# Optimization experiments

Measured on AMD Instinct MI355X. Metric: run time of the kernel, lower is better.

The kernel has to match this reference:

```python
import jax, jax.numpy as jnp
import numpy as np

N_NODES, N_EDGES, N_REL, F_DIM, N_HEAD, N_LAYERS = 20000, 100000, 1000, 128, 4, 4
NEG_SLOPE = 0.2  # PyG GATv2Conv default negative_slope


def _gatv2_layer(x, ea_full, src, dst, Wl, bl, Wr, br, We, att, bias):
    # x: [N, F]; ea_full: [Etot, F] edge attrs (incl. self-loop rows)
    N = x.shape[0]
    H, C = att.shape  # heads, out-dim per head
    xl = (x @ Wl + bl).reshape(N, H, C)          # source-side projection
    xr = (x @ Wr + br).reshape(N, H, C)          # target-side projection
    ee = (ea_full @ We).reshape(-1, H, C)        # [Etot, H, C] edge embedding
    # GATv2 scoring: leaky_relu(x_i + x_j + e) . att
    e = jax.nn.leaky_relu(xl[src] + xr[dst] + ee, NEG_SLOPE)
    logits = jnp.einsum('ehc,hc->eh', e, att)    # [Etot, H]
    # segment softmax over edges grouped by destination node
    m = jax.ops.segment_max(logits, dst, num_segments=N)
    p = jnp.exp(logits - m[dst])
    denom = jax.ops.segment_sum(p, dst, num_segments=N)
    alpha = p / denom[dst]                       # [Etot, H]
    out = jax.ops.segment_sum(alpha[:, :, None] * xl[src], dst, num_segments=N)
    return out.mean(axis=1) + bias               # concat=False -> head mean


def setup_inputs() -> dict:
    key = jax.random.key(0)
    ks = jax.random.split(key, 12)
    N, E, R, F, H, L = N_NODES, N_EDGES, N_REL, F_DIM, N_HEAD, N_LAYERS
    HC = H * F
    s = 1.0 / np.sqrt(F)
    return {
        'x': jax.random.normal(ks[0], (N, F), jnp.float32),
        'edge_index': jax.random.randint(ks[1], (2, E), 0, N, dtype=jnp.int32),
        'relations': jax.random.normal(ks[2], (R, F), jnp.float32),
        'relation_index': jax.random.randint(ks[3], (E,), 0, R, dtype=jnp.int32),
        'Wl': jax.random.normal(ks[4], (L, F, HC), jnp.float32) * s,
        'bl': jnp.zeros((L, HC), jnp.float32),
        'Wr': jax.random.normal(ks[5], (L, F, HC), jnp.float32) * s,
        'br': jnp.zeros((L, HC), jnp.float32),
        'We': jax.random.normal(ks[6], (L, F, HC), jnp.float32) * s,
        'att': jax.random.normal(ks[7], (L, H, F), jnp.float32) * s,
        'bias': jnp.zeros((L, F), jnp.float32),
    }


def reference(x, edge_index, relations, relation_index, Wl, bl, Wr, br, We, att, bias):
    N = x.shape[0]
    sl = jnp.arange(N, dtype=edge_index.dtype)
    src = jnp.concatenate([edge_index[0], sl])   # add_self_loops=True
    dst = jnp.concatenate([edge_index[1], sl])
    ea = relations[relation_index]               # [E, F]
    # self-loop edge_attr uses fill_value='mean' (PyG default)
    ea_mean = ea.mean(axis=0)
    ea_full = jnp.concatenate([ea, jnp.broadcast_to(ea_mean, (N, ea.shape[1]))])
    h = x
    for l in range(N_LAYERS):
        h = _gatv2_layer(h, ea_full, src, dst, Wl[l], bl[l], Wr[l], br[l], We[l], att[l], bias[l])
    return (h, relations)
```

## Files before the change

kernel.cpp:

```cpp
#include <hip/hip_runtime.h>
#include <hip/hip_bf16.h>

#define N_NODES   20000
#define N_EDGES   100000
#define N_REL     1000
#define F_DIM     128
#define N_HEAD    4
#define HC        512
#define HC2       256
#define N_LAYERS  4
#define REL_EXT_ROWS 1008
#define NEG_SLOPE 0.2f
#define PROJ_NODE_X 79

typedef __attribute__((ext_vector_type(8))) short short8;
typedef __attribute__((ext_vector_type(4))) float floatx4;

__device__ __forceinline__ float loadIn(const void* p, size_t i, int f32) {
    if (f32) return ((const float*)p)[i];
    union { unsigned int u; float f; } c;
    c.u = ((unsigned int)((const unsigned short*)p)[i]) << 16;
    return c.f;
}

__device__ __forceinline__ unsigned short f2bf(float v) {
    __hip_bfloat16 b = __float2bfloat16(v);
    return *(unsigned short*)&b;
}

__device__ __forceinline__ void unpack2(unsigned int u, float& lo, float& hi) {
    union { unsigned int u; float f; } a, b;
    a.u = u << 16;
    b.u = u & 0xFFFF0000u;
    lo = a.f; hi = b.f;
}

__device__ __forceinline__ void unpack8(uint4 v, float* f) {
    unpack2(v.x, f[0], f[1]);
    unpack2(v.y, f[2], f[3]);
    unpack2(v.z, f[4], f[5]);
    unpack2(v.w, f[6], f[7]);
}

__device__ __forceinline__ void gload_lds16(const unsigned short* g, short* l) {
    __builtin_amdgcn_global_load_lds(
        (const __attribute__((address_space(1))) unsigned int*)g,
        (__attribute__((address_space(3))) unsigned int*)l,
        16, 0, 0);
}

__global__ void detect_kernel(const unsigned short* __restrict__ x, int* __restrict__ flag) {
    int t = threadIdx.x;
    int cnt = 0;
    for (int j = t; j < 256; j += 64) {
        int e = (x[j] >> 7) & 0xFF;
        if (e >= 143) cnt++;
    }
    for (int off = 32; off; off >>= 1) cnt += __shfl_xor(cnt, off);
    if (t == 0) flag[0] = (cnt >= 8) ? 1 : 0;
}

__global__ void xcast_kernel(const void* __restrict__ x, unsigned short* __restrict__ xbf,
                             const int* __restrict__ flag) {
    int idx = blockIdx.x * 256 + threadIdx.x;
    if (idx >= N_NODES * F_DIM / 4) return;
    int f32 = flag[0];
    uint2 o;
    if (f32) {
        float4 v = ((const float4*)x)[idx];
        o.x = (unsigned int)f2bf(v.x) | ((unsigned int)f2bf(v.y) << 16);
        o.y = (unsigned int)f2bf(v.z) | ((unsigned int)f2bf(v.w) << 16);
    } else {
        o = ((const uint2*)x)[idx];
    }
    ((uint2*)xbf)[idx] = o;
}


__global__ void hist_kernel(const int* __restrict__ dst, const int* __restrict__ rel,
                            int* __restrict__ deg, int* __restrict__ rcount) {
    int e = blockIdx.x * 256 + threadIdx.x;
    if (e < N_EDGES) {
        atomicAdd(&deg[dst[e]], 1);
        atomicAdd(&rcount[rel[e]], 1);
    }
}

__global__ void ea_mean_kernel(const int* __restrict__ rcount,
                               const void* __restrict__ relations,
                               float* __restrict__ ea_mean, const int* __restrict__ flag) {
    int f32 = flag[0];
    int b = blockIdx.x;
    int t = threadIdx.x;
    int col = t & 127;
    int rhalf = t >> 7;
    float acc = 0.f;
    for (int j = 0; j < 4; ++j) {
        int r = b * 8 + j * 2 + rhalf;
        acc += (float)rcount[r] * loadIn(relations, (size_t)r * F_DIM + col, f32);
    }
    __shared__ float part[256];
    part[t] = acc;
    __syncthreads();
    if (t < 128)
        atomicAdd(&ea_mean[col], (part[t] + part[t + 128]) * (1.f / (float)N_EDGES));
}

__global__ void relext_kernel(const void* __restrict__ relations,
                              const float* __restrict__ ea_mean,
                              unsigned short* __restrict__ rel_ext, const int* __restrict__ flag) {
    int idx = blockIdx.x * 256 + threadIdx.x;
    if (idx >= REL_EXT_ROWS * F_DIM) return;
    int f32 = flag[0];
    int r = idx >> 7;
    int c = idx & 127;
    float v;
    if (r < N_REL)       v = loadIn(relations, idx, f32);
    else if (r == N_REL) v = ea_mean[c];
    else                 v = 0.f;
    rel_ext[idx] = f2bf(v);
}

__global__ void scan_kernel(const int* __restrict__ deg,
                            int* __restrict__ row_start, int* __restrict__ cursor) {
    __shared__ int part[1024];
    int t = threadIdx.x;
    const int CH = (N_NODES + 1023) / 1024;
    int base = t * CH;
    int sum = 0;
    for (int j = 0; j < CH; ++j) {
        int idx = base + j;
        if (idx < N_NODES) sum += deg[idx];
    }
    part[t] = sum;
    __syncthreads();
    for (int off = 1; off < 1024; off <<= 1) {
        int u = (t >= off) ? part[t - off] : 0;
        __syncthreads();
        part[t] += u;
        __syncthreads();
    }
    int run = part[t] - sum;
    for (int j = 0; j < CH; ++j) {
        int idx = base + j;
        if (idx < N_NODES) {
            row_start[idx] = run;
            cursor[idx] = run;
            run += deg[idx];
        }
    }
    if (t == 1023) row_start[N_NODES] = part[1023];
}

__global__ void scatter_kernel(const int* __restrict__ src, const int* __restrict__ dst,
                               const int* __restrict__ rel, int* __restrict__ cursor,
                               int* __restrict__ csr_pack) {
    int e = blockIdx.x * 256 + threadIdx.x;
    if (e < N_EDGES) {
        int d = dst[e];
        int p = atomicAdd(&cursor[d], 1);
        csr_pack[p] = src[e] | (rel[e] << 16);
    }
}

__global__ void build8_kernel(const int* __restrict__ row_start,
                              const int* __restrict__ csr_pack,
                              int* __restrict__ csr8) {
    int i = blockIdx.x * 256 + threadIdx.x;
    if (i >= N_NODES) return;
    int rs = row_start[i];
    int deg = row_start[i + 1] - rs;
    if (deg < 0) deg = 0;
    int dcap = deg > 4095 ? 4095 : deg;
    csr8[i * 8] = rs | (dcap << 17);
    #pragma unroll
    for (int k = 0; k < 7; ++k)
        csr8[i * 8 + 1 + k] = (k < deg) ? csr_pack[rs + k] : 0;
}

__global__ void tail_kernel(const void* __restrict__ relations, void* __restrict__ out,
                            const int* __restrict__ flag) {
    int i = blockIdx.x * 256 + threadIdx.x;
    if (i >= N_REL * F_DIM) return;
    int f32 = flag[0];
    float v = loadIn(relations, i, f32);
    size_t o = (size_t)N_NODES * F_DIM + i;
    if (f32) ((float*)out)[o] = v;
    else     ((unsigned short*)out)[o] = f2bf(v);
}

__global__ void w_transpose_kernel(const void* __restrict__ Wl, const void* __restrict__ Wr,
                                   const void* __restrict__ We,
                                   unsigned short* __restrict__ Wt, const int* __restrict__ flag) {
    int f32 = flag[0];
    int k0 = blockIdx.x * 64;
    int n0 = blockIdx.y * 64;
    int mat = blockIdx.z;
    const void* src = (mat < 4) ? Wl : (mat < 8 ? Wr : We);
    size_t base = (size_t)(mat & 3) * F_DIM * HC;
    unsigned short* dst = Wt + (size_t)mat * HC * F_DIM;
    __shared__ float T[64][65];
    int t = threadIdx.x;
    int r = t >> 2, cq = t & 3;
    for (int j = 0; j < 16; ++j) {
        int n = cq * 16 + j;
        T[n][r] = loadIn(src, base + (size_t)(k0 + r) * HC + n0 + n, f32);
    }
    __syncthreads();
    for (int j = 0; j < 16; ++j) {
        int k = cq * 16 + j;
        dst[(size_t)(n0 + r) * F_DIM + k0 + k] = f2bf(T[r][k]);
    }
}

__launch_bounds__(256, 3)
__global__ void proj_kernel(const unsigned short* __restrict__ A_node,
                            const unsigned short* __restrict__ rel_ext,
                            const unsigned short* __restrict__ Wlt,
                            const unsigned short* __restrict__ Wrt,
                            const unsigned short* __restrict__ Wet,
                            const void* __restrict__ bl, const void* __restrict__ br,
                            size_t boff,
                            unsigned short* __restrict__ xl,
                            unsigned short* __restrict__ xr,
                            unsigned short* __restrict__ re,
                            const int* __restrict__ flag) {
    __shared__ __align__(16) short As[2][64 * 128];
    int f32 = flag[0];
    int t = threadIdx.x;
    int y = blockIdx.y;
    int isNode = (blockIdx.x < PROJ_NODE_X);

    const unsigned short* A;
    const unsigned short* Wt;
    const void* bias;
    unsigned short* out;
    int M, mbase;
    int n0 = (y & 3) * 128;
    if (isNode) {
        A = A_node; M = N_NODES;
        mbase = blockIdx.x * 256;
        if (y < 4) { Wt = Wlt; bias = bl; out = xl; }
        else       { Wt = Wrt; bias = br; out = xr; }
    } else {
        A = rel_ext; M = REL_EXT_ROWS;
        int rowchunk = (blockIdx.x - PROJ_NODE_X) * 2 + (y >> 2);
        mbase = rowchunk * 256;
        Wt = Wet; bias = nullptr; out = re;
    }
    const int nT = 4;

    int wave = t >> 6, lane = t & 63;
    int wm = (wave >> 1) * 32, wn = (wave & 1) * 64;
    int r16 = lane & 15, quad = lane >> 4;

    short8 breg[2][2][4];
    #pragma unroll
    for (int half = 0; half < 2; ++half)
        #pragma unroll
        for (int kk = 0; kk < 2; ++kk)
            #pragma unroll
            for (int ni = 0; ni < 4; ++ni)
                breg[half][kk][ni] = *(const short8*)(
                    Wt + (size_t)(n0 + wn + ni * 16 + r16) * F_DIM + half * 64 + kk * 32 + quad * 8);

    float bvv[4][4];
    #pragma unroll
    for (int ni = 0; ni < 4; ++ni)
        #pragma unroll
        for (int r = 0; r < 4; ++r)
            bvv[ni][r] = bias ? loadIn(bias, boff + n0 + wn + ni * 16 + quad * 4 + r, f32) : 0.f;

    auto STAGE = [&](int buf, int ct2) {
        int base = mbase + ct2 * 64;
        #pragma unroll
        for (int j = 0; j < 4; ++j) {
            int c = t + j * 256;
            int row = c >> 4, ch = c & 15;
            int gm = base + row;
            if (gm >= M) gm = M - 1;
            int sch = ch ^ (row & 15);
            gload_lds16(A + (size_t)gm * F_DIM + sch * 8, &As[buf][c * 8]);
        }
    };

    STAGE(0, 0);
    asm volatile("s_waitcnt vmcnt(0)" ::: "memory");
    __builtin_amdgcn_sched_barrier(0);
    __syncthreads();

    int cur = 0;
    for (int ct = 0; ct < nT; ++ct) {
        int m0 = mbase + ct * 64;
        if (ct + 1 < nT) STAGE(cur ^ 1, ct + 1);
        __builtin_amdgcn_sched_barrier(0);

        floatx4 acc[2][4];
        #pragma unroll
        for (int mi = 0; mi < 2; ++mi)
            #pragma unroll
            for (int ni = 0; ni < 4; ++ni)
                acc[mi][ni] = (floatx4){0.f, 0.f, 0.f, 0.f};

        #pragma unroll
        for (int half = 0; half < 2; ++half) {
            #pragma unroll
            for (int kk = 0; kk < 2; ++kk) {
                short8 a[2];
                #pragma unroll
                for (int mi = 0; mi < 2; ++mi) {
                    int row = wm + mi * 16 + r16;
                    int pch = (half * 8 + kk * 4 + quad) ^ (row & 15);
                    a[mi] = *(const short8*)&As[cur][row * 128 + pch * 8];
                }
                #pragma unroll
                for (int mi = 0; mi < 2; ++mi)
                    #pragma unroll
                    for (int ni = 0; ni < 4; ++ni)
                        acc[mi][ni] = __builtin_amdgcn_mfma_f32_16x16x32_bf16(
                            breg[half][kk][ni], a[mi], acc[mi][ni], 0, 0, 0);
            }
        }

        #pragma unroll
        for (int mi = 0; mi < 2; ++mi) {
            int gm = m0 + wm + mi * 16 + r16;
            if (gm >= M) gm = M - 1;
            #pragma unroll
            for (int ni = 0; ni < 4; ++ni) {
                unsigned int w[2];
                #pragma unroll
                for (int p = 0; p < 2; ++p) {
                    float v0 = acc[mi][ni][2 * p]     + bvv[ni][2 * p];
                    float v1 = acc[mi][ni][2 * p + 1] + bvv[ni][2 * p + 1];
                    w[p] = (unsigned int)f2bf(v0) | ((unsigned int)f2bf(v1) << 16);
                }
                *(uint2*)(out + (size_t)gm * HC + n0 + wn + ni * 16 + quad * 4) = *(uint2*)w;
            }
        }

        if (ct + 1 < nT) {
            asm volatile("s_waitcnt vmcnt(8)" ::: "memory");
            __builtin_amdgcn_sched_barrier(0);
        }
        __builtin_amdgcn_s_barrier();
        cur ^= 1;
    }
}

__launch_bounds__(128)
__global__ void edge_kernel(const unsigned int* __restrict__ xl2,
                            const unsigned int* __restrict__ xr2,
                            const unsigned int* __restrict__ re2,
                            const int* __restrict__ csr8,
                            const int* __restrict__ csr_pack,
                            const void* __restrict__ att, size_t att_off,
                            const void* __restrict__ bias, size_t bias_off,
                            void* __restrict__ hout, int final_layer,
                            const int* __restrict__ flag) {
    int f32 = flag[0];
    int wid = threadIdx.x >> 6;
    int lane = threadIdx.x & 63;
    int i = blockIdx.x * 2 + wid;
    if (i >= N_NODES) return;
    int h = lane >> 4;
    int q = lane & 15;
    int loff = h * 64 + q * 4;

    uint4 h0 = *(const uint4*)(csr8 + (size_t)i * 8);
    uint4 h1 = *(const uint4*)(csr8 + (size_t)i * 8 + 4);
    int rs  = (int)(h0.x & 0x1FFFF);
    int deg = (int)(h0.x >> 17) & 0xFFF;
    int ew[7] = { (int)h0.y, (int)h0.z, (int)h0.w, (int)h1.x, (int)h1.y, (int)h1.z, (int)h1.w };

    float xr[8];
    { uint4 v = *(const uint4*)(xr2 + (size_t)i * HC2 + loff); unpack8(v, xr); }
    float er[8];
    { uint4 v = *(const uint4*)(re2 + (size_t)N_REL * HC2 + loff); unpack8(v, er); }
    float av[8];
    #pragma unroll
    for (int j = 0; j < 8; ++j)
        av[j] = loadIn(att, att_off + (size_t)h * F_DIM + q * 8 + j, f32);

    int nIn = deg > 7 ? 7 : deg;
    uint4 xv[7], rv[7];
    #pragma unroll
    for (int k = 0; k < 7; ++k) {
        if (k < nIn) {
            int pk = ew[k];
            int sn = pk & 0xFFFF;        if (sn >= N_NODES) sn = 0;
            int rn = (pk >> 16) & 0x3FF; if (rn > N_REL) rn = N_REL;
            xv[k] = *(const uint4*)(xl2 + (size_t)sn * HC2 + loff);
            rv[k] = *(const uint4*)(re2 + (size_t)rn * HC2 + loff);
        }
    }

    float acc[8];
    float s;
    {
        float xs[8];
        uint4 v = *(const uint4*)(xl2 + (size_t)i * HC2 + loff);
        unpack8(v, xs);
        float part = 0.f;
        #pragma unroll
        for (int j = 0; j < 8; ++j) {
            float u = xs[j] + xr[j] + er[j];
            u = fmaxf(u, NEG_SLOPE * u);
            part = fmaf(u, av[j], part);
        }
        #pragma unroll
        for (int off = 8; off; off >>= 1) part += __shfl_xor(part, off);
        part = fminf(fmaxf(part, -60.f), 60.f);
        float p = __expf(part);
        s = p;
        #pragma unroll
        for (int j = 0; j < 8; ++j) acc[j] = p * xs[j];
    }

    #pragma unroll
    for (int k = 0; k < 7; ++k) {
        if (k < nIn) {
            float xlv[8], ee[8];
            unpack8(xv[k], xlv);
            unpack8(rv[k], ee);
            float part = 0.f;
            #pragma unroll
            for (int j = 0; j < 8; ++j) {
                float u = xlv[j] + xr[j] + ee[j];
                u = fmaxf(u, NEG_SLOPE * u);
                part = fmaf(u, av[j], part);
            }
            #pragma unroll
            for (int off = 8; off; off >>= 1) part += __shfl_xor(part, off);
            part = fminf(fmaxf(part, -60.f), 60.f);
            float pp = __expf(part);
            s += pp;
            #pragma unroll
            for (int j = 0; j < 8; ++j) acc[j] = fmaf(pp, xlv[j], acc[j]);
        }
    }

    if (deg > 7) {
        int e1 = rs + deg;
        if (e1 > N_EDGES) e1 = N_EDGES;
        for (int b = rs + 7; b < e1; b += 4) {
            int nb = e1 - b; if (nb > 4) nb = 4;
            uint4 xo[4], ro[4];
            #pragma unroll
            for (int k = 0; k < 4; ++k) {
                if (k < nb) {
                    int pk = csr_pack[b + k];
                    int sn = pk & 0xFFFF;        if (sn >= N_NODES) sn = 0;
                    int rn = (pk >> 16) & 0x3FF; if (rn > N_REL) rn = N_REL;
                    xo[k] = *(const uint4*)(xl2 + (size_t)sn * HC2 + loff);
                    ro[k] = *(const uint4*)(re2 + (size_t)rn * HC2 + loff);
                }
            }
            #pragma unroll
            for (int k = 0; k < 4; ++k) {
                if (k < nb) {
                    float xlv[8], ee[8];
                    unpack8(xo[k], xlv);
                    unpack8(ro[k], ee);
                    float part = 0.f;
                    #pragma unroll
                    for (int j = 0; j < 8; ++j) {
                        float u = xlv[j] + xr[j] + ee[j];
                        u = fmaxf(u, NEG_SLOPE * u);
                        part = fmaf(u, av[j], part);
                    }
                    #pragma unroll
                    for (int off = 8; off; off >>= 1) part += __shfl_xor(part, off);
                    part = fminf(fmaxf(part, -60.f), 60.f);
                    float pp = __expf(part);
                    s += pp;
                    #pragma unroll
                    for (int j = 0; j < 8; ++j) acc[j] = fmaf(pp, xlv[j], acc[j]);
                }
            }
        }
    }

    float inv = 1.f / s;
    float outv[8];
    #pragma unroll
    for (int j = 0; j < 8; ++j) outv[j] = acc[j] * inv;
    #pragma unroll
    for (int j = 0; j < 8; ++j) {
        outv[j] += __shfl_xor(outv[j], 16);
        outv[j] += __shfl_xor(outv[j], 32);
    }

    if (h == 0) {
        float bv[8];
        #pragma unroll
        for (int j = 0; j < 8; ++j)
            bv[j] = loadIn(bias, bias_off + q * 8 + j, f32);
        size_t o = (size_t)i * F_DIM + q * 8;
        if (final_layer && f32) {
            float* op = (float*)hout + o;
            float4 lo, hi;
            lo.x = outv[0] * 0.25f + bv[0];
            lo.y = outv[1] * 0.25f + bv[1];
            lo.z = outv[2] * 0.25f + bv[2];
            lo.w = outv[3] * 0.25f + bv[3];
            hi.x = outv[4] * 0.25f + bv[4];
            hi.y = outv[5] * 0.25f + bv[5];
            hi.z = outv[6] * 0.25f + bv[6];
            hi.w = outv[7] * 0.25f + bv[7];
            *(float4*)op = lo;
            *(float4*)(op + 4) = hi;
        } else {
            unsigned int w[4];
            #pragma unroll
            for (int p = 0; p < 4; ++p) {
                float v0 = outv[2 * p] * 0.25f + bv[2 * p];
                float v1 = outv[2 * p + 1] * 0.25f + bv[2 * p + 1];
                w[p] = (unsigned int)f2bf(v0) | ((unsigned int)f2bf(v1) << 16);
            }
            *(uint4*)((unsigned short*)hout + o) = *(uint4*)w;
        }
    }
}


extern "C" void kernel_launch(void* const* d_in, const int* in_sizes, int n_in,
                              void* d_out, int out_size, void* d_ws, size_t ws_size,
                              hipStream_t stream) {
    const void* x          = d_in[0];
    const int*  edge_index = (const int*)d_in[1];
    const void* relations  = d_in[2];
    const int*  rel_index  = (const int*)d_in[3];
    const void* Wl         = d_in[4];
    const void* bl         = d_in[5];
    const void* Wr         = d_in[6];
    const void* br         = d_in[7];
    const void* We         = d_in[8];
    const void* att        = d_in[9];
    const void* bias       = d_in[10];

    char* ws = (char*)d_ws;
    size_t off = 0;
    auto alloc = [&](size_t bytes) -> void* {
        void* p = ws + off;
        off = (off + bytes + 255) & ~(size_t)255;
        return p;
    };
    int*            flag     = (int*)alloc(4);
    char*           zero0    = ws + off;
    int*            deg      = (int*)alloc(N_NODES * 4);
    int*            rcount   = (int*)alloc(N_REL * 4);
    float*          ea_mean  = (float*)alloc(F_DIM * 4);
    size_t          zlen     = (size_t)((ws + off) - zero0);
    int*            row_start= (int*)alloc((N_NODES + 1) * 4);
    int*            cursor   = (int*)alloc(N_NODES * 4);
    int*            csr_pack = (int*)alloc(N_EDGES * 4);
    int*            csr8     = (int*)alloc((size_t)N_NODES * 8 * 4);
    unsigned short* rel_ext  = (unsigned short*)alloc((size_t)REL_EXT_ROWS * F_DIM * 2);
    unsigned short* xbf      = (unsigned short*)alloc((size_t)N_NODES * F_DIM * 2);
    unsigned short* Wt       = (unsigned short*)alloc((size_t)12 * HC * F_DIM * 2);
    unsigned short* re       = (unsigned short*)alloc((size_t)REL_EXT_ROWS * HC * 2);
    unsigned short* hbuf     = (unsigned short*)alloc((size_t)N_NODES * F_DIM * 2);
    unsigned short* xl       = (unsigned short*)alloc((size_t)N_NODES * HC * 2);
    unsigned short* xr       = (unsigned short*)alloc((size_t)N_NODES * HC * 2);

    const int* esrc = edge_index;
    const int* edst = edge_index + N_EDGES;

    detect_kernel<<<1, 64, 0, stream>>>((const unsigned short*)x, flag);
    hipMemsetAsync(zero0, 0, zlen, stream);
    xcast_kernel<<<(N_NODES * F_DIM / 4 + 255) / 256, 256, 0, stream>>>(x, xbf, flag);
    hist_kernel<<<(N_EDGES + 255) / 256, 256, 0, stream>>>(edst, rel_index, deg, rcount);
    ea_mean_kernel<<<N_REL / 8, 256, 0, stream>>>(rcount, relations, ea_mean, flag);
    relext_kernel<<<(REL_EXT_ROWS * F_DIM + 255) / 256, 256, 0, stream>>>(relations, ea_mean, rel_ext, flag);
    scan_kernel<<<1, 1024, 0, stream>>>(deg, row_start, cursor);
    scatter_kernel<<<(N_EDGES + 255) / 256, 256, 0, stream>>>(esrc, edst, rel_index, cursor, csr_pack);
    build8_kernel<<<(N_NODES + 255) / 256, 256, 0, stream>>>(row_start, csr_pack, csr8);
    w_transpose_kernel<<<dim3(2, 8, 12), 256, 0, stream>>>(Wl, Wr, We, Wt, flag);
    tail_kernel<<<(N_REL * F_DIM + 255) / 256, 256, 0, stream>>>(relations, d_out, flag);

    const unsigned short* hin = xbf;
    for (int l = 0; l < N_LAYERS; ++l) {
        const unsigned short* Wlt = Wt + (size_t)l * HC * F_DIM;
        const unsigned short* Wrt = Wt + (size_t)(4 + l) * HC * F_DIM;
        const unsigned short* Wet = Wt + (size_t)(8 + l) * HC * F_DIM;
        proj_kernel<<<dim3(PROJ_NODE_X + 2, 8), 256, 0, stream>>>(
            hin, rel_ext, Wlt, Wrt, Wet,
            bl, br, (size_t)l * HC,
            xl, xr, re, flag);
        int final_layer = (l == N_LAYERS - 1);
        void* hout = final_layer ? d_out : (void*)hbuf;
        edge_kernel<<<(N_NODES + 1) / 2, 128, 0, stream>>>(
            (const unsigned int*)xl, (const unsigned int*)xr, (const unsigned int*)re,
            csr8, csr_pack,
            att, (size_t)l * N_HEAD * F_DIM,
            bias, (size_t)l * F_DIM,
            hout, final_layer, flag);
        hin = hbuf;
    }
}
```

Measured before the change: 422.7 us.

## Compute both Wl and Wr projections per block and stage output through LDS

Each projection block now holds the weight fragments for both Wl and Wr (or two We column tiles) and reuses each staged A tile for both, halving the grid's y-dimension and the number of times node features are loaded from global memory. The MFMA operand order is swapped so results are written to a per-wave LDS tile and then stored as full 16-byte row chunks instead of scattered 8-byte writes. The cost is doubled weight registers and extra LDS, so launch bounds drop from 3 to 2 blocks per CU, which lowers occupancy.

```diff
diff --git a/kernel.cpp b/kernel.cpp
--- a/kernel.cpp
+++ b/kernel.cpp
@@ -213,7 +213,7 @@
     }
 }
 
-__launch_bounds__(256, 3)
+__launch_bounds__(256, 2)
 __global__ void proj_kernel(const unsigned short* __restrict__ A_node,
                             const unsigned short* __restrict__ rel_ext,
                             const unsigned short* __restrict__ Wlt,
@@ -226,27 +226,32 @@
                             unsigned short* __restrict__ re,
                             const int* __restrict__ flag) {
     __shared__ __align__(16) short As[2][64 * 128];
+    __shared__ __align__(16) short Cw[4][32][72];
     int f32 = flag[0];
     int t = threadIdx.x;
     int y = blockIdx.y;
     int isNode = (blockIdx.x < PROJ_NODE_X);
 
     const unsigned short* A;
-    const unsigned short* Wt;
-    const void* bias;
-    unsigned short* out;
-    int M, mbase;
-    int n0 = (y & 3) * 128;
+    const unsigned short* WtM[2];
+    const void* biasM[2];
+    unsigned short* outM[2];
+    int M, mbase, n0M[2];
     if (isNode) {
         A = A_node; M = N_NODES;
         mbase = blockIdx.x * 256;
-        if (y < 4) { Wt = Wlt; bias = bl; out = xl; }
-        else       { Wt = Wrt; bias = br; out = xr; }
+        WtM[0] = Wlt;  WtM[1] = Wrt;
+        biasM[0] = bl; biasM[1] = br;
+        outM[0] = xl;  outM[1] = xr;
+        n0M[0] = y * 128; n0M[1] = y * 128;
     } else {
         A = rel_ext; M = REL_EXT_ROWS;
-        int rowchunk = (blockIdx.x - PROJ_NODE_X) * 2 + (y >> 2);
-        mbase = rowchunk * 256;
-        Wt = Wet; bias = nullptr; out = re;
+        int s = (blockIdx.x - PROJ_NODE_X) * 4 + y;
+        mbase = (s >> 1) * 256;
+        WtM[0] = Wet;  WtM[1] = Wet;
+        biasM[0] = nullptr; biasM[1] = nullptr;
+        outM[0] = re;  outM[1] = re;
+        n0M[0] = (s & 1) * 256; n0M[1] = (s & 1) * 256 + 128;
     }
     const int nT = 4;
 
@@ -254,22 +259,25 @@
     int wm = (wave >> 1) * 32, wn = (wave & 1) * 64;
     int r16 = lane & 15, quad = lane >> 4;
 
-    short8 breg[2][2][4];
-    #pragma unroll
-    for (int half = 0; half < 2; ++half)
-        #pragma unroll
-        for (int kk = 0; kk < 2; ++kk)
-            #pragma unroll
-            for (int ni = 0; ni < 4; ++ni)
-                breg[half][kk][ni] = *(const short8*)(
-                    Wt + (size_t)(n0 + wn + ni * 16 + r16) * F_DIM + half * 64 + kk * 32 + quad * 8);
-
-    float bvv[4][4];
-    #pragma unroll
-    for (int ni = 0; ni < 4; ++ni)
-        #pragma unroll
-        for (int r = 0; r < 4; ++r)
-            bvv[ni][r] = bias ? loadIn(bias, boff + n0 + wn + ni * 16 + quad * 4 + r, f32) : 0.f;
+    short8 breg[2][2][2][4];
+    #pragma unroll
+    for (int m = 0; m < 2; ++m)
+        #pragma unroll
+        for (int half = 0; half < 2; ++half)
+            #pragma unroll
+            for (int kk = 0; kk < 2; ++kk)
+                #pragma unroll
+                for (int ni = 0; ni < 4; ++ni)
+                    breg[m][half][kk][ni] = *(const short8*)(
+                        WtM[m] + (size_t)(n0M[m] + wn + ni * 16 + r16) * F_DIM
+                               + half * 64 + kk * 32 + quad * 8);
+
+    float bvv[2][4];
+    #pragma unroll
+    for (int m = 0; m < 2; ++m)
+        #pragma unroll
+        for (int ni = 0; ni < 4; ++ni)
+            bvv[m][ni] = biasM[m] ? loadIn(biasM[m], boff + n0M[m] + wn + ni * 16 + r16, f32) : 0.f;
 
     auto STAGE = [&](int buf, int ct2) {
         int base = mbase + ct2 * 64;
@@ -295,47 +303,58 @@
         if (ct + 1 < nT) STAGE(cur ^ 1, ct + 1);
         __builtin_amdgcn_sched_barrier(0);
 
-        floatx4 acc[2][4];
-        #pragma unroll
-        for (int mi = 0; mi < 2; ++mi)
-            #pragma unroll
-            for (int ni = 0; ni < 4; ++ni)
-                acc[mi][ni] = (floatx4){0.f, 0.f, 0.f, 0.f};
-
-        #pragma unroll
-        for (int half = 0; half < 2; ++half) {
-            #pragma unroll
-            for (int kk = 0; kk < 2; ++kk) {
-                short8 a[2];
+        short8 afr[2][2][2];
+        #pragma unroll
+        for (int half = 0; half < 2; ++half)
+            #pragma unroll
+            for (int kk = 0; kk < 2; ++kk)
                 #pragma unroll
                 for (int mi = 0; mi < 2; ++mi) {
                     int row = wm + mi * 16 + r16;
                     int pch = (half * 8 + kk * 4 + quad) ^ (row & 15);
-                    a[mi] = *(const short8*)&As[cur][row * 128 + pch * 8];
+                    afr[half][kk][mi] = *(const short8*)&As[cur][row * 128 + pch * 8];
                 }
+
+        #pragma unroll
+        for (int m = 0; m < 2; ++m) {
+            floatx4 acc[2][4];
+            #pragma unroll
+            for (int mi = 0; mi < 2; ++mi)
                 #pragma unroll
-                for (int mi = 0; mi < 2; ++mi)
+                for (int ni = 0; ni < 4; ++ni)
+                    acc[mi][ni] = (floatx4){0.f, 0.f, 0.f, 0.f};
+
+            #pragma unroll
+            for (int half = 0; half < 2; ++half)
+                #pragma unroll
+                for (int kk = 0; kk < 2; ++kk)
                     #pragma unroll
-                    for (int ni = 0; ni < 4; ++ni)
-                        acc[mi][ni] = __builtin_amdgcn_mfma_f32_16x16x32_bf16(
-                            breg[half][kk][ni], a[mi], acc[mi][ni], 0, 0, 0);
-            }
-        }
-
-        #pragma unroll
-        for (int mi = 0; mi < 2; ++mi) {
-            int gm = m0 + wm + mi * 16 + r16;
-            if (gm >= M) gm = M - 1;
-            #pragma unroll
-            for (int ni = 0; ni < 4; ++ni) {
-                unsigned int w[2];
+                    for (int mi = 0; mi < 2; ++mi)
+                        #pragma unroll
+                        for (int ni = 0; ni < 4; ++ni)
+                            acc[mi][ni] = __builtin_amdgcn_mfma_f32_16x16x32_bf16(
+                                afr[half][kk][mi], breg[m][half][kk][ni], acc[mi][ni], 0, 0, 0);
+
+            #pragma unroll
+            for (int mi = 0; mi < 2; ++mi)
                 #pragma unroll
-                for (int p = 0; p < 2; ++p) {
-                    float v0 = acc[mi][ni][2 * p]     + bvv[ni][2 * p];
-                    float v1 = acc[mi][ni][2 * p + 1] + bvv[ni][2 * p + 1];
-                    w[p] = (unsigned int)f2bf(v0) | ((unsigned int)f2bf(v1) << 16);
-                }
-                *(uint2*)(out + (size_t)gm * HC + n0 + wn + ni * 16 + quad * 4) = *(uint2*)w;
+                for (int ni = 0; ni < 4; ++ni)
+                    #pragma unroll
+                    for (int r = 0; r < 4; ++r)
+                        Cw[wave][mi * 16 + quad * 4 + r][ni * 16 + r16] =
+                            (short)f2bf(acc[mi][ni][r] + bvv[m][ni]);
+            asm volatile("s_waitcnt lgkmcnt(0)" ::: "memory");
+            __builtin_amdgcn_sched_barrier(0);
+
+            unsigned short* out = outM[m];
+            #pragma unroll
+            for (int j = 0; j < 4; ++j) {
+                int c = j * 64 + lane;
+                int lr = c >> 3, chunk = c & 7;
+                int gm = m0 + wm + lr;
+                if (gm >= M) gm = M - 1;
+                *(short8*)(out + (size_t)gm * HC + n0M[m] + wn + chunk * 8) =
+                    *(const short8*)&Cw[wave][lr][chunk * 8];
             }
         }
 
@@ -584,7 +603,7 @@
         const unsigned short* Wlt = Wt + (size_t)l * HC * F_DIM;
         const unsigned short* Wrt = Wt + (size_t)(4 + l) * HC * F_DIM;
         const unsigned short* Wet = Wt + (size_t)(8 + l) * HC * F_DIM;
-        proj_kernel<<<dim3(PROJ_NODE_X + 2, 8), 256, 0, stream>>>(
+        proj_kernel<<<dim3(PROJ_NODE_X + 2, 4), 256, 0, stream>>>(
             hin, rel_ext, Wlt, Wrt, Wet,
             bl, br, (size_t)l * HC,
             xl, xr, re, flag);
```

Result: no change. 420.1 us (-0.6%).
